# Optimization experiments

Measured on AMD Instinct MI355X. Metric: run time of the kernel, lower is better.

Reference implementation:

```python
import jax, jax.numpy as jnp
import numpy as np

N, E, F_IN, EDIM, H = 50000, 1600000, 128, 16, 4
C1, C2, G, NCLS = 32, 8, 64, 10
NEG_SLOPE = 0.2


def setup_inputs() -> dict:
    key = jax.random.key(0)
    ks = jax.random.split(key, 20)
    s = 0.1
    inp = {
        "x": jax.random.normal(ks[0], (N, F_IN), jnp.float32),
        "edge_index": jax.random.randint(ks[1], (2, E), 0, N, dtype=jnp.int32),
        "edge_attr": jax.random.normal(ks[2], (E, EDIM), jnp.float32),
        "batch": jnp.sort(jax.random.randint(ks[3], (N,), 0, G, dtype=jnp.int32)),
        # layer 1 params (PyG GATConv: shared lin for src/dst, no lin bias)
        "W1": jax.random.normal(ks[4], (F_IN, H * C1), jnp.float32) * s,
        "as1": jax.random.normal(ks[5], (H, C1), jnp.float32) * s,
        "ad1": jax.random.normal(ks[6], (H, C1), jnp.float32) * s,
        "We1": jax.random.normal(ks[7], (EDIM, H * C1), jnp.float32) * s,
        "ae1": jax.random.normal(ks[8], (H, C1), jnp.float32) * s,
        "b1": jnp.zeros((H * C1,), jnp.float32),
        # layer 2 params
        "W2": jax.random.normal(ks[9], (H * C1, H * C2), jnp.float32) * s,
        "as2": jax.random.normal(ks[10], (H, C2), jnp.float32) * s,
        "ad2": jax.random.normal(ks[11], (H, C2), jnp.float32) * s,
        "We2": jax.random.normal(ks[12], (EDIM, H * C2), jnp.float32) * s,
        "ae2": jax.random.normal(ks[13], (H, C2), jnp.float32) * s,
        "b2": jnp.zeros((H * C2,), jnp.float32),
        # final linear
        "Wfc": jax.random.normal(ks[14], (H * C2, NCLS), jnp.float32) * s,
        "bfc": jnp.zeros((NCLS,), jnp.float32),
    }
    return inp


def _add_self_loops(src, dst, edge_attr):
    # PyG default: add_self_loops=True, fill_value='mean' (mean of incoming edge attrs)
    deg = jax.ops.segment_sum(jnp.ones((E,), jnp.float32), dst, num_segments=N)
    loop_attr = jax.ops.segment_sum(edge_attr, dst, num_segments=N) / jnp.maximum(deg, 1.0)[:, None]
    loop = jnp.arange(N, dtype=src.dtype)
    return (jnp.concatenate([src, loop]), jnp.concatenate([dst, loop]),
            jnp.concatenate([edge_attr, loop_attr], axis=0))


def _gat_layer(x, src, dst, ea, W, a_src, a_dst, We, a_e, b, heads, ch):
    n = x.shape[0]
    h = (x @ W).reshape(n, heads, ch)                 # [N,H,C]
    he = (ea @ We).reshape(-1, heads, ch)             # [Ef,H,C]
    al_src = jnp.einsum('nhc,hc->nh', h, a_src)       # [N,H]
    al_dst = jnp.einsum('nhc,hc->nh', h, a_dst)
    al_e = jnp.einsum('ehc,hc->eh', he, a_e)          # [Ef,H]
    alpha = al_src[src] + al_dst[dst] + al_e
    alpha = jax.nn.leaky_relu(alpha, NEG_SLOPE)
    # edge softmax grouped by destination node
    amax = jax.ops.segment_max(alpha, dst, num_segments=n)
    alpha = jnp.exp(alpha - amax[dst])
    denom = jax.ops.segment_sum(alpha, dst, num_segments=n)
    alpha = alpha / (denom[dst] + 1e-16)
    out = jax.ops.segment_sum(h[src] * alpha[..., None], dst, num_segments=n)  # [N,H,C]
    return out.reshape(n, heads * ch) + b


def reference(x, edge_index, edge_attr, batch, W1, as1, ad1, We1, ae1, b1,
              W2, as2, ad2, We2, ae2, b2, Wfc, bfc):
    src, dst = edge_index[0], edge_index[1]
    src, dst, ea = _add_self_loops(src, dst, edge_attr)
    h = jax.nn.relu(_gat_layer(x, src, dst, ea, W1, as1, ad1, We1, ae1, b1, H, C1))
    h = jax.nn.relu(_gat_layer(h, src, dst, ea, W2, as2, ad2, We2, ae2, b2, H, C2))
    # global mean pool over graphs
    cnt = jax.ops.segment_sum(jnp.ones((N,), jnp.float32), batch, num_segments=G)
    pooled = jax.ops.segment_sum(h, batch, num_segments=G) / jnp.maximum(cnt, 1.0)[:, None]
    return pooled @ Wfc + bfc
```

## Files before the change

kernel.cpp:

```cpp
#include <hip/hip_runtime.h>
#include <hip/hip_fp16.h>
#include <math.h>

typedef float4 f4;
#define NEG_SLOPE 0.2f
#define NBMAX 1024
#define BIN_CHUNK 8192

union alerec { float4 f; __half2 h[4]; };

__global__ void k_prep(const float* __restrict__ We1, const float* __restrict__ ae1,
                       const float* __restrict__ We2, const float* __restrict__ ae2,
                       float* __restrict__ M) {
    int t = threadIdx.x;
    if (t >= 128) return;
    int sel = t >> 6, i = t & 63, d = i >> 2, h = i & 3;
    const float* W  = sel ? We2 : We1;
    const float* ae = sel ? ae2 : ae1;
    int C = sel ? 8 : 32, ncol = sel ? 32 : 128;
    float s = 0.f;
    for (int c = 0; c < C; ++c) s += W[d * ncol + h * C + c] * ae[h * C + c];
    M[sel * 64 + d * 4 + h] = s;
}

__global__ __launch_bounds__(256) void k_bhist(const int* __restrict__ ei,
                                               int* __restrict__ bcnt, int E, int NB) {
    __shared__ int hist[NBMAX];
    for (int i = threadIdx.x; i < NB; i += 256) hist[i] = 0;
    __syncthreads();
    int stride = gridDim.x * 256;
    for (int e = blockIdx.x * 256 + threadIdx.x; e < E; e += stride)
        atomicAdd(&hist[ei[E + e] >> 6], 1);
    __syncthreads();
    for (int i = threadIdx.x; i < NB; i += 256) {
        int h = hist[i];
        if (h) atomicAdd(&bcnt[i], h);
    }
}

__global__ void k_bscan(const int* __restrict__ bcnt, int* __restrict__ bprefix,
                        int* __restrict__ bcursor, int NB) {
    __shared__ int ts[NBMAX];
    int t = threadIdx.x;
    ts[t] = (t < NB) ? bcnt[t] : 0;
    __syncthreads();
    for (int off = 1; off < 1024; off <<= 1) {
        int v = (t >= off) ? ts[t - off] : 0;
        __syncthreads();
        ts[t] += v;
        __syncthreads();
    }
    int excl = (t == 0) ? 0 : ts[t - 1];
    if (t <= NB) {
        bprefix[t] = excl;
        if (t < NB) bcursor[t] = excl;
    }
}

__global__ __launch_bounds__(256) void k_bin(const int* __restrict__ ei,
                                             const float* __restrict__ ea,
                                             const float* __restrict__ Mbuf,
                                             int* __restrict__ bcursor,
                                             int* __restrict__ binned_meta,
                                             float4* __restrict__ binned_ale,
                                             int E, int NB) {
    __shared__ int hist[NBMAX], base[NBMAX], cur[NBMAX];
    __shared__ float Ms[128];
    if (threadIdx.x < 128) Ms[threadIdx.x] = Mbuf[threadIdx.x];
    for (int i = threadIdx.x; i < NB; i += 256) { hist[i] = 0; cur[i] = 0; }
    __syncthreads();
    int e0 = blockIdx.x * BIN_CHUNK;
    int e1 = min(e0 + BIN_CHUNK, E);
    for (int e = e0 + threadIdx.x; e < e1; e += 256)
        atomicAdd(&hist[ei[E + e] >> 6], 1);
    __syncthreads();
    for (int i = threadIdx.x; i < NB; i += 256) {
        int h = hist[i];
        if (h) base[i] = atomicAdd(&bcursor[i], h);
    }
    __syncthreads();
    for (int e = e0 + threadIdx.x; e < e1; e += 256) {
        int sr = ei[e], d = ei[E + e];
        const f4* row = (const f4*)(ea + (size_t)e * 16);
        f4 r0 = row[0], r1 = row[1], r2 = row[2], r3 = row[3];
        float a[16] = { r0.x, r0.y, r0.z, r0.w, r1.x, r1.y, r1.z, r1.w,
                        r2.x, r2.y, r2.z, r2.w, r3.x, r3.y, r3.z, r3.w };
        float s10 = 0.f, s11 = 0.f, s12 = 0.f, s13 = 0.f;
        float s20 = 0.f, s21 = 0.f, s22 = 0.f, s23 = 0.f;
#pragma unroll
        for (int dd = 0; dd < 16; ++dd) {
            float av = a[dd];
            s10 += av * Ms[dd * 4 + 0]; s11 += av * Ms[dd * 4 + 1];
            s12 += av * Ms[dd * 4 + 2]; s13 += av * Ms[dd * 4 + 3];
            s20 += av * Ms[64 + dd * 4 + 0]; s21 += av * Ms[64 + dd * 4 + 1];
            s22 += av * Ms[64 + dd * 4 + 2]; s23 += av * Ms[64 + dd * 4 + 3];
        }
        int b = d >> 6;
        int loc = base[b] + atomicAdd(&cur[b], 1);
        binned_meta[loc] = sr | ((d & 63) << 16);
        alerec r;
        r.h[0] = __floats2half2_rn(s10, s11); r.h[1] = __floats2half2_rn(s12, s13);
        r.h[2] = __floats2half2_rn(s20, s21); r.h[3] = __floats2half2_rn(s22, s23);
        binned_ale[loc] = r.f;
    }
}

__global__ __launch_bounds__(256) void k_csr(const int* __restrict__ binned_meta,
                                             const float4* __restrict__ binned_ale,
                                             const int* __restrict__ bprefix,
                                             int* __restrict__ offsets,
                                             int* __restrict__ csr_src,
                                             float2* __restrict__ csr_ale1,
                                             float2* __restrict__ csr_ale2,
                                             int N, int E, int NB) {
    __shared__ int nhist[64], noff[65];
    int b = blockIdx.x;
    if (threadIdx.x < 64) nhist[threadIdx.x] = 0;
    __syncthreads();
    int lo = bprefix[b], hi = bprefix[b + 1];
    for (int s = lo + threadIdx.x; s < hi; s += 256)
        atomicAdd(&nhist[(binned_meta[s] >> 16) & 63], 1);
    __syncthreads();
    if (threadIdx.x == 0) {
        int run = 0;
        for (int i = 0; i < 64; ++i) { noff[i] = run; run += nhist[i]; }
        noff[64] = run;
    }
    __syncthreads();
    int nlo = b << 6;
    int nbn = min(64, N - nlo);
    if (threadIdx.x < nbn) offsets[nlo + threadIdx.x] = lo + noff[threadIdx.x];
    if (b == NB - 1 && threadIdx.x == 0) offsets[N] = E;
    if (threadIdx.x < 64) nhist[threadIdx.x] = 0;
    __syncthreads();
    for (int s = lo + threadIdx.x; s < hi; s += 256) {
        int m = binned_meta[s];
        float4 rec = binned_ale[s];
        int dl = (m >> 16) & 63;
        int slot = lo + noff[dl] + atomicAdd(&nhist[dl], 1);
        csr_src[slot] = m & 0xFFFF;
        csr_ale1[slot] = make_float2(rec.x, rec.y);
        csr_ale2[slot] = make_float2(rec.z, rec.w);
    }
}

template<int NOUT, int ROWS>
__global__ __launch_bounds__(256) void k_gemm(const float* __restrict__ X,
                                              const float* __restrict__ W,
                                              __half* __restrict__ Hout, int N) {
    __shared__ __align__(16) float xs[ROWS][128];
    int row0 = blockIdx.x * ROWS;
    int tid = threadIdx.x;
    constexpr int NF4 = ROWS * 32;
    const f4* x4 = (const f4*)X;
    for (int i = tid; i < NF4; i += 256) {
        int r = i >> 5, k4 = i & 31;
        f4 v;
        if (row0 + r < N) v = x4[(size_t)(row0 + r) * 32 + k4];
        else { v.x = v.y = v.z = v.w = 0.f; }
        ((f4*)&xs[r][0])[k4] = v;
    }
    __syncthreads();
    constexpr int GRP = 256 / NOUT;
    constexpr int PR  = ROWS / GRP;
    int col = tid % NOUT, rg = tid / NOUT;
    float acc[PR];
#pragma unroll
    for (int r = 0; r < PR; ++r) acc[r] = 0.f;
    for (int k = 0; k < 128; ++k) {
        float w = W[k * NOUT + col];
#pragma unroll
        for (int r = 0; r < PR; ++r) acc[r] += xs[rg + r * GRP][k] * w;
    }
#pragma unroll
    for (int r = 0; r < PR; ++r) {
        int row = row0 + rg + r * GRP;
        if (row < N) Hout[(size_t)row * NOUT + col] = __float2half(acc[r]);
    }
}

template<int C>
__global__ void k_al(const __half* __restrict__ Hm, const float* __restrict__ as_,
                     const float* __restrict__ ad_, float* __restrict__ als,
                     float* __restrict__ ald, int N) {
    int idx = blockIdx.x * 256 + threadIdx.x;
    int n = idx >> 2, h = idx & 3;
    if (n >= N) return;
    constexpr int CH = C / 4;
    const __half2* h2p = (const __half2*)(Hm + (size_t)n * C + h * CH);
    float a = 0.f, b = 0.f;
#pragma unroll
    for (int c = 0; c < CH / 2; ++c) {
        float2 v = __half22float2(h2p[c]);
        a += v.x * as_[h * CH + 2 * c] + v.y * as_[h * CH + 2 * c + 1];
        b += v.x * ad_[h * CH + 2 * c] + v.y * ad_[h * CH + 2 * c + 1];
    }
    als[n * 4 + h] = a;
    ald[n * 4 + h] = b;
}

__global__ __launch_bounds__(256) void k_alpha_node(const float2* __restrict__ csr_ale,
                                                    __half* __restrict__ alpha_csr,
                                                    const int* __restrict__ csr_src,
                                                    const float* __restrict__ als,
                                                    const float* __restrict__ ald,
                                                    const int* __restrict__ offsets,
                                                    float* __restrict__ rden,
                                                    float* __restrict__ selfa, int N) {
    int n = (blockIdx.x * 256 + threadIdx.x) >> 6;
    int lane = threadIdx.x & 63;
    if (n >= N) return;
    int j = lane >> 2, h = lane & 3;
    int s0 = offsets[n], s1 = offsets[n + 1];
    float aldn = ald[n * 4 + h];
    float den = 0.f, asum = 0.f;
    const __half* aleh = (const __half*)csr_ale;
    for (int base = s0; base < s1; base += 16) {
        int s = base + j;
        if (s < s1) {
            int src = csr_src[s];
            float ale = __half2float(aleh[(size_t)s * 4 + h]);
            float v = als[src * 4 + h] + aldn + ale;
            v = (v > 0.f) ? v : NEG_SLOPE * v;
            float e = __expf(v);
            alpha_csr[s * 4 + h] = __float2half(e);
            den += e; asum += ale;
        }
    }
    den  += __shfl_xor(den, 4);  den  += __shfl_xor(den, 8);
    den  += __shfl_xor(den, 16); den  += __shfl_xor(den, 32);
    asum += __shfl_xor(asum, 4);  asum += __shfl_xor(asum, 8);
    asum += __shfl_xor(asum, 16); asum += __shfl_xor(asum, 32);
    if (j == 0) {
        float rdeg = 1.f / fmaxf((float)(s1 - s0), 1.f);
        float v = als[n * 4 + h] + aldn + asum * rdeg;
        v = (v > 0.f) ? v : NEG_SLOPE * v;
        float es = __expf(v);
        selfa[n * 4 + h] = es;
        rden[n * 4 + h] = 1.f / (den + es + 1e-16f);
    }
}

__global__ __launch_bounds__(256) void k_aggf128(const __half* __restrict__ h16,
                                                 const __half* __restrict__ alpha16,
                                                 const float* __restrict__ rden,
                                                 const float* __restrict__ selfa,
                                                 const int* __restrict__ offsets,
                                                 const int* __restrict__ csr_src,
                                                 const float* __restrict__ bias,
                                                 float* __restrict__ Out, int N) {
    int n = (blockIdx.x * 256 + threadIdx.x) >> 6;
    int lane = threadIdx.x & 63;
    if (n >= N) return;
    int hd = lane >> 4;
    int s0 = offsets[n], s1 = offsets[n + 1];
    const __half2* H2 = (const __half2*)h16;
    float acc0 = 0.f, acc1 = 0.f;
    int e1 = s1 - 1;
    for (int s = s0; s < s1; s += 8) {
        int srck[8]; float ak[8]; __half2 hvk[8];
#pragma unroll
        for (int k = 0; k < 8; ++k) {
            int sk = min(s + k, e1);
            srck[k] = csr_src[sk];
            ak[k] = (s + k <= e1) ? __half2float(alpha16[(size_t)sk * 4 + hd]) : 0.f;
        }
#pragma unroll
        for (int k = 0; k < 8; ++k) hvk[k] = H2[(size_t)srck[k] * 64 + lane];
#pragma unroll
        for (int k = 0; k < 8; ++k) {
            float2 f = __half22float2(hvk[k]);
            acc0 = fmaf(ak[k], f.x, acc0);
            acc1 = fmaf(ak[k], f.y, acc1);
        }
    }
    float sa = selfa[n * 4 + hd];
    float2 hn = __half22float2(H2[(size_t)n * 64 + lane]);
    acc0 = fmaf(sa, hn.x, acc0);
    acc1 = fmaf(sa, hn.y, acc1);
    float rd = rden[n * 4 + hd];
    float2 bv = ((const float2*)bias)[lane];
    float2 o;
    o.x = fmaxf(fmaf(acc0, rd, bv.x), 0.f);
    o.y = fmaxf(fmaf(acc1, rd, bv.y), 0.f);
    ((float2*)Out)[(size_t)n * 64 + lane] = o;
}

__global__ __launch_bounds__(256) void k_aggf32(const __half* __restrict__ h16,
                                                const __half* __restrict__ alpha16,
                                                const float* __restrict__ rden,
                                                const float* __restrict__ selfa,
                                                const int* __restrict__ offsets,
                                                const int* __restrict__ csr_src,
                                                const float* __restrict__ bias,
                                                float* __restrict__ Out, int N) {
    int n = (blockIdx.x * 256 + threadIdx.x) >> 6;
    int lane = threadIdx.x & 63;
    if (n >= N) return;
    int j = lane >> 4;
    int p = lane & 15;
    int hd = p >> 2;
    int s0 = offsets[n], s1 = offsets[n + 1];
    const __half2* H2 = (const __half2*)h16;
    float acc0 = 0.f, acc1 = 0.f;
    int e1 = s1 - 1;
    for (int s = s0 + j; s < s1; s += 8) {
        int sA = s;
        int sB = min(s + 4, e1);
        int srcA = csr_src[sA], srcB = csr_src[sB];
        float aA = __half2float(alpha16[(size_t)sA * 4 + hd]);
        float aB = (s + 4 <= e1) ? __half2float(alpha16[(size_t)sB * 4 + hd]) : 0.f;
        __half2 hA = H2[(size_t)srcA * 16 + p];
        __half2 hB = H2[(size_t)srcB * 16 + p];
        float2 fA = __half22float2(hA), fB = __half22float2(hB);
        acc0 = fmaf(aA, fA.x, acc0); acc1 = fmaf(aA, fA.y, acc1);
        acc0 = fmaf(aB, fB.x, acc0); acc1 = fmaf(aB, fB.y, acc1);
    }
    acc0 += __shfl_xor(acc0, 16); acc0 += __shfl_xor(acc0, 32);
    acc1 += __shfl_xor(acc1, 16); acc1 += __shfl_xor(acc1, 32);
    if (j == 0) {
        float sa = selfa[n * 4 + hd];
        float2 hn = __half22float2(H2[(size_t)n * 16 + p]);
        acc0 = fmaf(sa, hn.x, acc0);
        acc1 = fmaf(sa, hn.y, acc1);
        float rd = rden[n * 4 + hd];
        float2 bv = ((const float2*)bias)[p];
        float2 o;
        o.x = fmaxf(fmaf(acc0, rd, bv.x), 0.f);
        o.y = fmaxf(fmaf(acc1, rd, bv.y), 0.f);
        ((float2*)Out)[(size_t)n * 16 + p] = o;
    }
}

__global__ void k_gbound(const int* __restrict__ batch, int* __restrict__ gstart, int N, int G) {
    int g = threadIdx.x;
    if (g > G) return;
    int lo = 0, hi = N;
    while (lo < hi) {
        int mid = (lo + hi) >> 1;
        if (batch[mid] < g) lo = mid + 1; else hi = mid;
    }
    gstart[g] = lo;
}

__global__ __launch_bounds__(256) void k_pool_grp(const float* __restrict__ out2,
                                                  const int* __restrict__ gstart,
                                                  float* __restrict__ pooled, int G) {
    __shared__ float red[8][32];
    int g = blockIdx.x;
    int t = threadIdx.x, c = t & 31, r = t >> 5;
    int s0 = gstart[g], s1 = gstart[g + 1];
    float acc = 0.f;
    for (int n = s0 + r; n < s1; n += 8) acc += out2[(size_t)n * 32 + c];
    red[r][c] = acc;
    __syncthreads();
    if (r == 0) {
        float s = red[0][c];
#pragma unroll
        for (int i = 1; i < 8; ++i) s += red[i][c];
        pooled[g * 32 + c] = s;
    }
}

__global__ void k_final(const float* __restrict__ pooled, const int* __restrict__ gstart,
                        const float* __restrict__ Wfc, const float* __restrict__ bfc,
                        float* __restrict__ out) {
    int t = threadIdx.x;
    if (t >= 640) return;
    int g = t / 10, cls = t % 10;
    float rc = 1.f / fmaxf((float)(gstart[g + 1] - gstart[g]), 1.f);
    float acc = bfc[cls];
    for (int c = 0; c < 32; ++c) acc += pooled[g * 32 + c] * rc * Wfc[c * 10 + cls];
    out[g * 10 + cls] = acc;
}

extern "C" void kernel_launch(void* const* d_in, const int* in_sizes, int n_in,
                              void* d_out, int out_size, void* d_ws, size_t ws_size,
                              hipStream_t stream) {
    const float* x    = (const float*)d_in[0];
    const int*   ei   = (const int*)  d_in[1];
    const float* ea   = (const float*)d_in[2];
    const int*   batch= (const int*)  d_in[3];
    const float* W1   = (const float*)d_in[4];
    const float* as1  = (const float*)d_in[5];
    const float* ad1  = (const float*)d_in[6];
    const float* We1  = (const float*)d_in[7];
    const float* ae1  = (const float*)d_in[8];
    const float* b1   = (const float*)d_in[9];
    const float* W2   = (const float*)d_in[10];
    const float* as2  = (const float*)d_in[11];
    const float* ad2  = (const float*)d_in[12];
    const float* We2  = (const float*)d_in[13];
    const float* ae2  = (const float*)d_in[14];
    const float* b2   = (const float*)d_in[15];
    const float* Wfc  = (const float*)d_in[16];
    const float* bfc  = (const float*)d_in[17];
    float* out = (float*)d_out;

    const int N  = in_sizes[3];
    const int E  = in_sizes[1] / 2;
    const int G  = 64;
    const int NB = (N + 63) >> 6;

    char* w = (char*)d_ws;
    size_t off = 0;
    auto alloc = [&](size_t bytes) -> void* {
        void* p = w + off;
        off = (off + bytes + 255) & ~(size_t)255;
        return p;
    };
    int*    bcnt       = (int*)   alloc((size_t)NBMAX * 4);
    int*    bprefix    = (int*)   alloc((size_t)(NBMAX + 1) * 4);
    int*    bcursor    = (int*)   alloc((size_t)NBMAX * 4);
    int*    offsets    = (int*)   alloc((size_t)(N + 1) * 4);
    int*    binned_meta= (int*)   alloc((size_t)E * 4);
    float4* binned_ale = (float4*)alloc((size_t)E * 16);
    int*    csr_src    = (int*)   alloc((size_t)E * 4);
    float2* csr_ale1   = (float2*)alloc((size_t)E * 8);
    float2* csr_ale2   = (float2*)alloc((size_t)E * 8);
    float*  Mbuf       = (float*) alloc(128 * 4);
    __half* h16        = (__half*)alloc((size_t)N * 128 * 2);
    float*  out1       = (float*) alloc((size_t)N * 128 * 4);
    float*  als        = (float*) alloc((size_t)N * 4 * 4);
    float*  ald        = (float*) alloc((size_t)N * 4 * 4);
    float*  rden       = (float*) alloc((size_t)N * 4 * 4);
    float*  selfa      = (float*) alloc((size_t)N * 4 * 4);
    int*    gstart     = (int*)   alloc((G + 1) * 4);
    float*  pooled     = (float*) alloc(G * 32 * 4);
    __half* alpha_csr  = (__half*)binned_ale;
    float*  out2 = out1;

    const int nb4 = (N + 3) / 4;

    hipMemsetAsync(bcnt, 0, (size_t)NBMAX * 4, stream);

    k_prep<<<1, 128, 0, stream>>>(We1, ae1, We2, ae2, Mbuf);
    k_bhist<<<128, 256, 0, stream>>>(ei, bcnt, E, NB);
    k_bscan<<<1, 1024, 0, stream>>>(bcnt, bprefix, bcursor, NB);
    k_bin<<<(E + BIN_CHUNK - 1) / BIN_CHUNK, 256, 0, stream>>>(ei, ea, Mbuf, bcursor,
                                                               binned_meta, binned_ale, E, NB);
    k_csr<<<NB, 256, 0, stream>>>(binned_meta, binned_ale, bprefix, offsets,
                                  csr_src, csr_ale1, csr_ale2, N, E, NB);
    k_gbound<<<1, 128, 0, stream>>>(batch, gstart, N, G);

    k_gemm<128, 16><<<(N + 15) / 16, 256, 0, stream>>>(x, W1, h16, N);
    k_al<128><<<(N * 4 + 255) / 256, 256, 0, stream>>>(h16, as1, ad1, als, ald, N);
    k_alpha_node<<<nb4, 256, 0, stream>>>(csr_ale1, alpha_csr, csr_src, als, ald, offsets, rden, selfa, N);
    k_aggf128<<<nb4, 256, 0, stream>>>(h16, alpha_csr, rden, selfa, offsets, csr_src, b1, out1, N);

    k_gemm<32, 64><<<(N + 63) / 64, 256, 0, stream>>>(out1, W2, h16, N);
    k_al<32><<<(N * 4 + 255) / 256, 256, 0, stream>>>(h16, as2, ad2, als, ald, N);
    k_alpha_node<<<nb4, 256, 0, stream>>>(csr_ale2, alpha_csr, csr_src, als, ald, offsets, rden, selfa, N);
    k_aggf32<<<nb4, 256, 0, stream>>>(h16, alpha_csr, rden, selfa, offsets, csr_src, b2, out2, N);

    k_pool_grp<<<G, 256, 0, stream>>>(out2, gstart, pooled, G);
    k_final<<<1, 640, 0, stream>>>(pooled, gstart, Wfc, bfc, out);
}
```

Before: 421.1 us.

## Split edge-attr projection into coalesced kernel and gather it in CSR build

Moves the edge_attr-by-M projection out of the binning kernel into a separate fully parallel kernel that writes per-edge half-precision attention terms in original edge order. The bin kernel now only scatters an 8-byte (src, local dst | edge id) record instead of a 4-byte meta plus a 16-byte record, and the CSR kernel gathers the attention terms by edge id. The aim is to cut scattered write traffic and raise occupancy for the heavy edge_attr read. In exchange it adds a kernel launch, an extra intermediate array pass, and random gathers in k_csr.

```diff
diff --git a/kernel.cpp b/kernel.cpp
--- a/kernel.cpp
+++ b/kernel.cpp
@@ -7,7 +7,7 @@
 #define NBMAX 1024
 #define BIN_CHUNK 8192
 
-union alerec { float4 f; __half2 h[4]; };
+union h4pack { float2 f; __half2 h[2]; };
 
 __global__ void k_prep(const float* __restrict__ We1, const float* __restrict__ ae1,
                        const float* __restrict__ We2, const float* __restrict__ ae2,
@@ -57,16 +57,38 @@
     }
 }
 
-__global__ __launch_bounds__(256) void k_bin(const int* __restrict__ ei,
-                                             const float* __restrict__ ea,
-                                             const float* __restrict__ Mbuf,
-                                             int* __restrict__ bcursor,
-                                             int* __restrict__ binned_meta,
-                                             float4* __restrict__ binned_ale,
-                                             int E, int NB) {
-    __shared__ int hist[NBMAX], base[NBMAX], cur[NBMAX];
+__global__ void k_ale_lin(const float* __restrict__ ea, const float* __restrict__ Mbuf,
+                          __half* __restrict__ ale1_e, __half* __restrict__ ale2_e, int E) {
     __shared__ float Ms[128];
     if (threadIdx.x < 128) Ms[threadIdx.x] = Mbuf[threadIdx.x];
+    __syncthreads();
+    int e = blockIdx.x * 256 + threadIdx.x;
+    if (e >= E) return;
+    const f4* row = (const f4*)(ea + (size_t)e * 16);
+    f4 r0 = row[0], r1 = row[1], r2 = row[2], r3 = row[3];
+    float a[16] = { r0.x, r0.y, r0.z, r0.w, r1.x, r1.y, r1.z, r1.w,
+                    r2.x, r2.y, r2.z, r2.w, r3.x, r3.y, r3.z, r3.w };
+    float s10 = 0.f, s11 = 0.f, s12 = 0.f, s13 = 0.f;
+    float s20 = 0.f, s21 = 0.f, s22 = 0.f, s23 = 0.f;
+#pragma unroll
+    for (int dd = 0; dd < 16; ++dd) {
+        float av = a[dd];
+        s10 += av * Ms[dd * 4 + 0]; s11 += av * Ms[dd * 4 + 1];
+        s12 += av * Ms[dd * 4 + 2]; s13 += av * Ms[dd * 4 + 3];
+        s20 += av * Ms[64 + dd * 4 + 0]; s21 += av * Ms[64 + dd * 4 + 1];
+        s22 += av * Ms[64 + dd * 4 + 2]; s23 += av * Ms[64 + dd * 4 + 3];
+    }
+    h4pack p1, p2;
+    p1.h[0] = __floats2half2_rn(s10, s11); p1.h[1] = __floats2half2_rn(s12, s13);
+    p2.h[0] = __floats2half2_rn(s20, s21); p2.h[1] = __floats2half2_rn(s22, s23);
+    ((float2*)ale1_e)[e] = p1.f;
+    ((float2*)ale2_e)[e] = p2.f;
+}
+
+__global__ __launch_bounds__(256) void k_bin(const int* __restrict__ ei,
+                                             int* __restrict__ bcursor,
+                                             int2* __restrict__ binned, int E, int NB) {
+    __shared__ int hist[NBMAX], base[NBMAX], cur[NBMAX];
     for (int i = threadIdx.x; i < NB; i += 256) { hist[i] = 0; cur[i] = 0; }
     __syncthreads();
     int e0 = blockIdx.x * BIN_CHUNK;
@@ -81,32 +103,15 @@
     __syncthreads();
     for (int e = e0 + threadIdx.x; e < e1; e += 256) {
         int sr = ei[e], d = ei[E + e];
-        const f4* row = (const f4*)(ea + (size_t)e * 16);
-        f4 r0 = row[0], r1 = row[1], r2 = row[2], r3 = row[3];
-        float a[16] = { r0.x, r0.y, r0.z, r0.w, r1.x, r1.y, r1.z, r1.w,
-                        r2.x, r2.y, r2.z, r2.w, r3.x, r3.y, r3.z, r3.w };
-        float s10 = 0.f, s11 = 0.f, s12 = 0.f, s13 = 0.f;
-        float s20 = 0.f, s21 = 0.f, s22 = 0.f, s23 = 0.f;
-#pragma unroll
-        for (int dd = 0; dd < 16; ++dd) {
-            float av = a[dd];
-            s10 += av * Ms[dd * 4 + 0]; s11 += av * Ms[dd * 4 + 1];
-            s12 += av * Ms[dd * 4 + 2]; s13 += av * Ms[dd * 4 + 3];
-            s20 += av * Ms[64 + dd * 4 + 0]; s21 += av * Ms[64 + dd * 4 + 1];
-            s22 += av * Ms[64 + dd * 4 + 2]; s23 += av * Ms[64 + dd * 4 + 3];
-        }
         int b = d >> 6;
         int loc = base[b] + atomicAdd(&cur[b], 1);
-        binned_meta[loc] = sr | ((d & 63) << 16);
-        alerec r;
-        r.h[0] = __floats2half2_rn(s10, s11); r.h[1] = __floats2half2_rn(s12, s13);
-        r.h[2] = __floats2half2_rn(s20, s21); r.h[3] = __floats2half2_rn(s22, s23);
-        binned_ale[loc] = r.f;
-    }
-}
-
-__global__ __launch_bounds__(256) void k_csr(const int* __restrict__ binned_meta,
-                                             const float4* __restrict__ binned_ale,
+        binned[loc] = make_int2(sr, ((d & 63) << 26) | e);
+    }
+}
+
+__global__ __launch_bounds__(256) void k_csr(const int2* __restrict__ binned,
+                                             const float2* __restrict__ ale1_e,
+                                             const float2* __restrict__ ale2_e,
                                              const int* __restrict__ bprefix,
                                              int* __restrict__ offsets,
                                              int* __restrict__ csr_src,
@@ -119,7 +124,7 @@
     __syncthreads();
     int lo = bprefix[b], hi = bprefix[b + 1];
     for (int s = lo + threadIdx.x; s < hi; s += 256)
-        atomicAdd(&nhist[(binned_meta[s] >> 16) & 63], 1);
+        atomicAdd(&nhist[(binned[s].y >> 26) & 63], 1);
     __syncthreads();
     if (threadIdx.x == 0) {
         int run = 0;
@@ -134,13 +139,15 @@
     if (threadIdx.x < 64) nhist[threadIdx.x] = 0;
     __syncthreads();
     for (int s = lo + threadIdx.x; s < hi; s += 256) {
-        int m = binned_meta[s];
-        float4 rec = binned_ale[s];
-        int dl = (m >> 16) & 63;
+        int2 r = binned[s];
+        int dl = (r.y >> 26) & 63;
+        int eid = r.y & 0x03FFFFFF;
+        float2 a1 = ale1_e[eid];
+        float2 a2 = ale2_e[eid];
         int slot = lo + noff[dl] + atomicAdd(&nhist[dl], 1);
-        csr_src[slot] = m & 0xFFFF;
-        csr_ale1[slot] = make_float2(rec.x, rec.y);
-        csr_ale2[slot] = make_float2(rec.z, rec.w);
+        csr_src[slot] = r.x;
+        csr_ale1[slot] = a1;
+        csr_ale2[slot] = a2;
     }
 }
 
@@ -413,8 +420,9 @@
     int*    bprefix    = (int*)   alloc((size_t)(NBMAX + 1) * 4);
     int*    bcursor    = (int*)   alloc((size_t)NBMAX * 4);
     int*    offsets    = (int*)   alloc((size_t)(N + 1) * 4);
-    int*    binned_meta= (int*)   alloc((size_t)E * 4);
-    float4* binned_ale = (float4*)alloc((size_t)E * 16);
+    int2*   binned     = (int2*)  alloc((size_t)E * 8);
+    __half* ale1_e     = (__half*)alloc((size_t)E * 4 * 2);
+    __half* ale2_e     = (__half*)alloc((size_t)E * 4 * 2);
     int*    csr_src    = (int*)   alloc((size_t)E * 4);
     float2* csr_ale1   = (float2*)alloc((size_t)E * 8);
     float2* csr_ale2   = (float2*)alloc((size_t)E * 8);
@@ -427,9 +435,10 @@
     float*  selfa      = (float*) alloc((size_t)N * 4 * 4);
     int*    gstart     = (int*)   alloc((G + 1) * 4);
     float*  pooled     = (float*) alloc(G * 32 * 4);
-    __half* alpha_csr  = (__half*)binned_ale;
+    __half* alpha_csr  = (__half*)binned;
     float*  out2 = out1;
 
+    const int eb  = (E + 255) / 256;
     const int nb4 = (N + 3) / 4;
 
     hipMemsetAsync(bcnt, 0, (size_t)NBMAX * 4, stream);
@@ -437,10 +446,10 @@
     k_prep<<<1, 128, 0, stream>>>(We1, ae1, We2, ae2, Mbuf);
     k_bhist<<<128, 256, 0, stream>>>(ei, bcnt, E, NB);
     k_bscan<<<1, 1024, 0, stream>>>(bcnt, bprefix, bcursor, NB);
-    k_bin<<<(E + BIN_CHUNK - 1) / BIN_CHUNK, 256, 0, stream>>>(ei, ea, Mbuf, bcursor,
-                                                               binned_meta, binned_ale, E, NB);
-    k_csr<<<NB, 256, 0, stream>>>(binned_meta, binned_ale, bprefix, offsets,
-                                  csr_src, csr_ale1, csr_ale2, N, E, NB);
+    k_ale_lin<<<eb, 256, 0, stream>>>(ea, Mbuf, ale1_e, ale2_e, E);
+    k_bin<<<(E + BIN_CHUNK - 1) / BIN_CHUNK, 256, 0, stream>>>(ei, bcursor, binned, E, NB);
+    k_csr<<<NB, 256, 0, stream>>>(binned, (const float2*)ale1_e, (const float2*)ale2_e,
+                                  bprefix, offsets, csr_src, csr_ale1, csr_ale2, N, E, NB);
     k_gbound<<<1, 128, 0, stream>>>(batch, gstart, N, G);
 
     k_gemm<128, 16><<<(N + 15) / 16, 256, 0, stream>>>(x, W1, h16, N);
```

After: 426.6 us. Within noise of the previous version (+1.3%).
